# Kernel tuning notes

Hardware: AMD Instinct MI355X
Metric: run time of the kernel (lower is better)

The kernel has to match this reference:

```python
import jax, jax.numpy as jnp
import numpy as np

N_WORD = 50000
N_DOC = 10000
E_WW = 800000
E_WD = 320000


def _sage(h_src, h_dst, src, dst, n_dst, W_self, W_neigh, b):
    # DGL SAGEConv('mean'): fc_self(h_dst) + fc_neigh(mean_{u in N(v)} h_u) + bias
    ones = jnp.ones((src.shape[0],), dtype=h_src.dtype)
    deg = jax.ops.segment_sum(ones, dst, num_segments=n_dst)            # [n_dst]
    agg = jax.ops.segment_sum(h_src[src], dst, num_segments=n_dst)      # [n_dst, d]
    mean = agg / jnp.maximum(deg, 1.0)[:, None]                          # zero for isolated
    return h_dst @ W_self + mean @ W_neigh + b


def _layer(xw, xd, edges, Ws, Wn, b):
    (ww_s, ww_d, wwr_s, wwr_d, wd_s, wd_d, wdr_s, wdr_d) = edges
    # relations targeting 'word': word2word, word2wordr, word2documentr
    h_ww = _sage(xw, xw, ww_s, ww_d, N_WORD, Ws[0], Wn[0], b[0])
    h_wwr = _sage(xw, xw, wwr_s, wwr_d, N_WORD, Ws[1], Wn[1], b[1])
    h_wdr = _sage(xd, xw, wdr_s, wdr_d, N_WORD, Ws[3], Wn[3], b[3])
    # relation targeting 'document': word2document
    h_wd = _sage(xw, xd, wd_s, wd_d, N_DOC, Ws[2], Wn[2], b[2])
    # HeteroGraphConv aggregate='stack' then torch.sum(dim=1) == sum over relations; then relu
    return jax.nn.relu(h_ww + h_wwr + h_wdr), jax.nn.relu(h_wd)


def setup_inputs() -> dict:
    key = jax.random.key(0)
    ks = jax.random.split(key, 20)
    d_in, d_h = 256, 128
    inp = {
        "x_word": jax.random.normal(ks[0], (N_WORD, d_in), jnp.float32),
        "x_doc": jax.random.normal(ks[1], (N_DOC, d_in), jnp.float32),
        "ww_src": jax.random.randint(ks[2], (E_WW,), 0, N_WORD, jnp.int32),
        "ww_dst": jax.random.randint(ks[3], (E_WW,), 0, N_WORD, jnp.int32),
        "wwr_src": jax.random.randint(ks[4], (E_WW,), 0, N_WORD, jnp.int32),
        "wwr_dst": jax.random.randint(ks[5], (E_WW,), 0, N_WORD, jnp.int32),
        "wd_src": jax.random.randint(ks[6], (E_WD,), 0, N_WORD, jnp.int32),
        "wd_dst": jax.random.randint(ks[7], (E_WD,), 0, N_DOC, jnp.int32),
        "wdr_src": jax.random.randint(ks[8], (E_WD,), 0, N_DOC, jnp.int32),
        "wdr_dst": jax.random.randint(ks[9], (E_WD,), 0, N_WORD, jnp.int32),
        "Wself1": jax.random.normal(ks[10], (4, d_in, d_h), jnp.float32) * (1.0 / np.sqrt(d_in)),
        "Wneigh1": jax.random.normal(ks[11], (4, d_in, d_h), jnp.float32) * (1.0 / np.sqrt(d_in)),
        "b1": jnp.zeros((4, d_h), jnp.float32),
        "Wself2": jax.random.normal(ks[12], (4, d_h, d_h), jnp.float32) * (1.0 / np.sqrt(d_h)),
        "Wneigh2": jax.random.normal(ks[13], (4, d_h, d_h), jnp.float32) * (1.0 / np.sqrt(d_h)),
        "b2": jnp.zeros((4, d_h), jnp.float32),
        "lin_w": jax.random.normal(ks[14], (1, d_h), jnp.float32) * (1.0 / np.sqrt(d_h)),
        "lin_b": jnp.ones((1,), jnp.float32),
    }
    return inp


def reference(x_word, x_doc, ww_src, ww_dst, wwr_src, wwr_dst, wd_src, wd_dst,
              wdr_src, wdr_dst, Wself1, Wneigh1, b1, Wself2, Wneigh2, b2, lin_w, lin_b):
    edges = (ww_src, ww_dst, wwr_src, wwr_dst, wd_src, wd_dst, wdr_src, wdr_dst)
    xw, xd = _layer(x_word, x_doc, edges, Wself1, Wneigh1, b1)
    xw, xd = _layer(xw, xd, edges, Wself2, Wneigh2, b2)
    out_w = jax.nn.sigmoid(xw @ lin_w.T + lin_b)  # [N_WORD, 1]
    out_d = jax.nn.sigmoid(xd @ lin_w.T + lin_b)  # [N_DOC, 1]
    return out_w, out_d
```

## Files before the change

### kernel.cpp

```cpp
#include <hip/hip_runtime.h>
#include <math.h>

#define N_WORD 50000
#define N_DOC  10000
#define E_WW   800000
#define E_WD   320000
#define D_IN   256
#define D_H    128

#define NPB    256
#define NBK_W  196
#define NBK_D  40
#define BKT    (3 * NBK_W + NBK_D)
#define EPB    8192
#define NBLK_WW 98
#define NBLK_WD 40
#define NBLK_TOT (2 * NBLK_WW + 2 * NBLK_WD)
#define PACK_BLKS 145

#define CAP_WW  4736
#define CAP_WDR 2176
#define CAP_WD  8960

#define WSTRIP ((N_WORD + 63) / 64)
#define DSTRIP ((N_DOC + 63) / 64)
#define NSTRIP (WSTRIP + DSTRIP)

typedef __attribute__((ext_vector_type(8))) short short8;
typedef __attribute__((ext_vector_type(4))) float f32x4;

__device__ inline unsigned short f2bf(float f) {
  unsigned u = __float_as_uint(f);
  u = (u + 0x7fffu + ((u >> 16) & 1u)) >> 16;
  return (unsigned short)u;
}

__device__ inline float bflo(unsigned u) { return __uint_as_float(u << 16); }
__device__ inline float bfhi(unsigned u) { return __uint_as_float(u & 0xffff0000u); }

struct G6 { const short* B[6]; unsigned short* C[6]; };

template <int ABF, int K>
__device__ void gemm_body(const void* __restrict__ Aw, const void* __restrict__ Ad,
                          const G6& g, int blk) {
  constexpr int KT = K >> 5;
  int wid = threadIdx.x >> 6, lane = threadIdx.x & 63;
  const void* A; int M, row0, h0, h1;
  if (blk < WSTRIP) { A = Aw; M = N_WORD; row0 = blk << 6; h0 = 0; h1 = 4; }
  else { A = Ad; M = N_DOC; row0 = (blk - WSTRIP) << 6; h0 = 4; h1 = 6; }
  int r = lane & 15, quad = lane >> 4;
  int m0 = row0 + wid * 16;
  int mA = m0 + r; if (mA >= M) mA = M - 1;
  short8 afr[KT];
  if (ABF) {
    const short* ap = (const short*)A + (size_t)mA * K + quad * 8;
#pragma unroll
    for (int kt = 0; kt < KT; ++kt) afr[kt] = *(const short8*)(ap + kt * 32);
  } else {
    const float* ap = (const float*)A + (size_t)mA * K + quad * 8;
#pragma unroll
    for (int kt = 0; kt < KT; ++kt) {
      float4 a0 = *(const float4*)(ap + kt * 32);
      float4 a1 = *(const float4*)(ap + kt * 32 + 4);
      short8 v;
      v[0] = (short)f2bf(a0.x); v[1] = (short)f2bf(a0.y);
      v[2] = (short)f2bf(a0.z); v[3] = (short)f2bf(a0.w);
      v[4] = (short)f2bf(a1.x); v[5] = (short)f2bf(a1.y);
      v[6] = (short)f2bf(a1.z); v[7] = (short)f2bf(a1.w);
      afr[kt] = v;
    }
  }
  for (int h = h0; h < h1; ++h) {
    const short* Bp = g.B[h];
    f32x4 acc[8];
#pragma unroll
    for (int nt = 0; nt < 8; ++nt) acc[nt] = (f32x4){0.f, 0.f, 0.f, 0.f};
#pragma unroll
    for (int kt = 0; kt < KT; ++kt) {
      const short* bbase = Bp + ((size_t)kt * 4096) + lane * 8;
#pragma unroll
      for (int nt = 0; nt < 8; ++nt) {
        short8 bf = *(const short8*)(bbase + (size_t)nt * 512);
        acc[nt] = __builtin_amdgcn_mfma_f32_16x16x32_bf16(afr[kt], bf, acc[nt], 0, 0, 0);
      }
    }
    unsigned short* C = g.C[h];
#pragma unroll
    for (int nt = 0; nt < 8; ++nt)
#pragma unroll
      for (int rr = 0; rr < 4; ++rr) {
        int row = m0 + quad * 4 + rr;
        if (row < M) C[(size_t)row * 128 + nt * 16 + r] = f2bf(acc[nt][rr]);
      }
  }
}

__global__ __launch_bounds__(256) void prep_kernel(
    const float* __restrict__ Ws1, const float* __restrict__ Wn1,
    const float* __restrict__ Ws2, const float* __restrict__ Wn2,
    short* __restrict__ Bp1, short* __restrict__ Bp2,
    const float* __restrict__ b1, const float* __restrict__ b2,
    float* __restrict__ bs1, float* __restrict__ bs2, int* __restrict__ bcnt,
    unsigned* __restrict__ zA, unsigned* __restrict__ zB,
    unsigned* __restrict__ zC, unsigned* __restrict__ zD) {
  int b = blockIdx.x;
  if (b == PACK_BLKS) {
    for (int i = threadIdx.x; i < BKT; i += 256) bcnt[i] = 0;
    if (threadIdx.x < 64) {
      zA[(size_t)N_WORD * 64 + threadIdx.x] = 0;
      zB[(size_t)N_WORD * 64 + threadIdx.x] = 0;
      zC[(size_t)N_WORD * 64 + threadIdx.x] = 0;
      zD[(size_t)N_DOC * 64 + threadIdx.x] = 0;
    }
    return;
  }
  int tid = b * 256 + threadIdx.x;
  const int L1T = 6 * 4096;
  const int L2T = 6 * 2048;
  if (tid >= L1T + L2T) {
    int t = tid - (L1T + L2T);
    if (t < 128) bs1[t] = b1[t] + b1[128 + t] + b1[384 + t];
    else if (t < 256) { int u = t - 128; bs2[u] = b2[u] + b2[128 + u] + b2[384 + u]; }
    return;
  }
  const float *src0, *src1 = nullptr, *src2 = nullptr;
  short* dstp;
  int kt, nt, lane;
  if (tid < L1T) {
    int mat = tid / 4096, rem = tid % 4096;
    kt = rem / 512; nt = (rem / 64) % 8; lane = rem % 64;
    const int W1 = 256 * 128;
    if (mat == 0) { src0 = Ws1; src1 = Ws1 + W1; src2 = Ws1 + 3 * W1; }
    else if (mat <= 4) src0 = Wn1 + (size_t)(mat - 1) * W1;
    else src0 = Ws1 + 2 * W1;
    dstp = Bp1 + (size_t)mat * W1 + ((size_t)(kt * 8 + nt) * 64 + lane) * 8;
  } else {
    int t2 = tid - L1T;
    int mat = t2 / 2048, rem = t2 % 2048;
    kt = rem / 512; nt = (rem / 64) % 8; lane = rem % 64;
    const int W2 = 128 * 128;
    if (mat == 0) { src0 = Ws2; src1 = Ws2 + W2; src2 = Ws2 + 3 * W2; }
    else if (mat <= 4) src0 = Wn2 + (size_t)(mat - 1) * W2;
    else src0 = Ws2 + 2 * W2;
    dstp = Bp2 + (size_t)mat * W2 + ((size_t)(kt * 8 + nt) * 64 + lane) * 8;
  }
  int n = nt * 16 + (lane & 15);
  int kb = kt * 32 + (lane >> 4) * 8;
  short8 v;
#pragma unroll
  for (int j = 0; j < 8; ++j) {
    float f = src0[(size_t)(kb + j) * 128 + n];
    if (src1) f += src1[(size_t)(kb + j) * 128 + n] + src2[(size_t)(kb + j) * 128 + n];
    v[j] = (short)f2bf(f);
  }
  *(short8*)dstp = v;
}

__device__ inline void rel_map(int b, const int* wwd, const int* wwrd, const int* wdrd,
                               const int* wdd, const int*& dst, int& E, int& gbase, int& lb) {
  if (b < NBLK_WW) { dst = wwd; E = E_WW; gbase = 0; lb = b; }
  else if (b < 2 * NBLK_WW) { dst = wwrd; E = E_WW; gbase = NBK_W; lb = b - NBLK_WW; }
  else if (b < 2 * NBLK_WW + NBLK_WD) { dst = wdrd; E = E_WD; gbase = 2 * NBK_W; lb = b - 2 * NBLK_WW; }
  else { dst = wdd; E = E_WD; gbase = 3 * NBK_W; lb = b - 2 * NBLK_WW - NBLK_WD; }
}

struct BinLDS {
  unsigned buf[EPB];
  int hist[NBK_W];
  int lofs[NBK_W];
  int gofs[NBK_W];
  int lcur[NBK_W];
  int sm[256];
};

__global__ __launch_bounds__(256, 4) void bin_gemm1(
    const int* wws, const int* wwd, const int* wwrs, const int* wwrd,
    const int* wdrs, const int* wdrd, const int* wds, const int* wdd,
    int* bcnt, unsigned* st_ww, unsigned* st_wwr, unsigned* st_wdr, unsigned* st_wd,
    const float* __restrict__ Aw, const float* __restrict__ Ad, G6 g) {
  __shared__ BinLDS L;
  int b = blockIdx.x;
  if (b >= NBLK_TOT) {
    gemm_body<0, 256>(Aw, Ad, g, b - NBLK_TOT);
    return;
  }
  const int* dst; int E, gbase, lb;
  rel_map(b, wwd, wwrd, wdrd, wdd, dst, E, gbase, lb);
  const int* src; unsigned* st; int cap;
  if (b < NBLK_WW) { src = wws; st = st_ww; cap = CAP_WW; }
  else if (b < 2 * NBLK_WW) { src = wwrs; st = st_wwr; cap = CAP_WW; }
  else if (b < 2 * NBLK_WW + NBLK_WD) { src = wdrs; st = st_wdr; cap = CAP_WDR; }
  else { src = wds; st = st_wd; cap = CAP_WD; }
  int tid = threadIdx.x;
  int e0 = lb * EPB;
  int ecnt = E - e0; if (ecnt > EPB) ecnt = EPB;
  if (tid < NBK_W) L.hist[tid] = 0;
  __syncthreads();
  int dcache[EPB / 256];
#pragma unroll
  for (int k = 0; k < EPB / 256; ++k) {
    int i = e0 + k * 256 + tid;
    int d = (i < E) ? dst[i] : -1;
    dcache[k] = d;
    if (d >= 0) atomicAdd(&L.hist[d >> 8], 1);
  }
  __syncthreads();
  {
    int v = (tid < NBK_W) ? L.hist[tid] : 0;
    L.sm[tid] = v;
    __syncthreads();
    for (int o = 1; o < 256; o <<= 1) {
      int add = (tid >= o) ? L.sm[tid - o] : 0;
      __syncthreads();
      L.sm[tid] += add;
      __syncthreads();
    }
    if (tid < NBK_W) {
      int ex = L.sm[tid] - v;
      L.lofs[tid] = ex;
      L.lcur[tid] = ex;
      int base = v ? atomicAdd(&bcnt[gbase + tid], v) : 0;
      L.gofs[tid] = (int)((size_t)tid * cap) + base - ex;
    }
  }
  __syncthreads();
#pragma unroll
  for (int k = 0; k < EPB / 256; ++k) {
    int d = dcache[k];
    if (d >= 0) {
      int i = e0 + k * 256 + tid;
      int bk = d >> 8;
      int p = atomicAdd(&L.lcur[bk], 1);
      L.buf[p] = ((unsigned)bk << 24) | ((unsigned)(d & 255) << 16) |
                 (unsigned)(src[i] & 0xFFFF);
    }
  }
  __syncthreads();
#pragma unroll
  for (int k = 0; k < EPB / 256; ++k) {
    int p = k * 256 + tid;
    if (p < ecnt) {
      unsigned e = L.buf[p];
      st[L.gofs[e >> 24] + p] = e & 0x00FFFFFFu;
    }
  }
}

struct CSRB {
  const unsigned *st_ww, *st_wwr, *st_wdr, *st_wd;
  unsigned short *c_ww, *c_wwr, *c_wdr, *c_wd;
  int *rp_ww, *rp_wwr, *rp_wdr, *rp_wd;
  const int* bcnt;
};

__global__ __launch_bounds__(256) void place_kernel(CSRB q) {
  __shared__ int cnt[256], off[256], sm[256];
  int g = blockIdx.x;
  const unsigned* st; unsigned short* csr; int* rp; int relFirst, relLast, n, cap, Etot;
  if (g < NBK_W)            { st = q.st_ww;  csr = q.c_ww;  rp = q.rp_ww;  relFirst = 0;         relLast = NBK_W - 1;     n = N_WORD; cap = CAP_WW;  Etot = E_WW; }
  else if (g < 2 * NBK_W)   { st = q.st_wwr; csr = q.c_wwr; rp = q.rp_wwr; relFirst = NBK_W;     relLast = 2 * NBK_W - 1; n = N_WORD; cap = CAP_WW;  Etot = E_WW; }
  else if (g < 3 * NBK_W)   { st = q.st_wdr; csr = q.c_wdr; rp = q.rp_wdr; relFirst = 2 * NBK_W; relLast = 3 * NBK_W - 1; n = N_WORD; cap = CAP_WDR; Etot = E_WD; }
  else                      { st = q.st_wd;  csr = q.c_wd;  rp = q.rp_wd;  relFirst = 3 * NBK_W; relLast = BKT - 1;       n = N_DOC;  cap = CAP_WD;  Etot = E_WD; }
  int cb = g - relFirst;
  int tid = threadIdx.x;
  int v = (tid < cb) ? q.bcnt[relFirst + tid] : 0;
  sm[tid] = v;
  __syncthreads();
  for (int o = 128; o > 0; o >>= 1) {
    if (tid < o) sm[tid] += sm[tid + o];
    __syncthreads();
  }
  int bstart = sm[0];
  if (g == relLast && tid == 0) rp[n] = Etot;
  __syncthreads();
  int node_base = cb << 8;
  int node_cnt = n - node_base; if (node_cnt > NPB) node_cnt = NPB;
  int ecnt = q.bcnt[g];
  const unsigned* w = st + (size_t)cb * cap;
  cnt[tid] = 0;
  __syncthreads();
  for (int j = tid; j < ecnt; j += 256) atomicAdd(&cnt[w[j] >> 16], 1);
  __syncthreads();
  int c = cnt[tid];
  sm[tid] = c;
  __syncthreads();
  for (int o = 1; o < 256; o <<= 1) {
    int add = (tid >= o) ? sm[tid - o] : 0;
    __syncthreads();
    sm[tid] += add;
    __syncthreads();
  }
  int ex = sm[tid] - c;
  off[tid] = ex;
  if (tid < node_cnt) rp[node_base + tid] = bstart + ex;
  __syncthreads();
  for (int j = tid; j < ecnt; j += 256) {
    unsigned e = w[j];
    int p = atomicAdd(&off[e >> 16], 1);
    csr[bstart + p] = (unsigned short)(e & 0xFFFFu);
  }
}

__global__ __launch_bounds__(256, 6) void gemm2_kernel(
    const void* __restrict__ Aw, const void* __restrict__ Ad, G6 g) {
  gemm_body<1, 128>(Aw, Ad, g, blockIdx.x);
}

__device__ inline void accum_rel4(const uint4* __restrict__ Y,
                                  const unsigned short* __restrict__ csr,
                                  int beg, int end, int lane, int r, int g,
                                  int zrow, float* __restrict__ f) {
  int deg = end - beg;
  if (deg <= 0) return;
  float a[8];
#pragma unroll
  for (int i = 0; i < 8; ++i) a[i] = 0.f;
  for (int base = beg; base < end; base += 64) {
    int cnt = end - base; if (cnt > 64) cnt = 64;
    int ld = base + lane; if (ld >= end) ld = end - 1;
    int idx = csr[ld];
    for (int j = 0; j < cnt; j += 16) {
      uint4 u[4];
#pragma unroll
      for (int t = 0; t < 4; ++t) {
        int e = j + (t << 2) + g;
        int sel = (e < cnt) ? e : 0;
        int sv = __shfl(idx, sel, 64);
        int s = (e < cnt) ? sv : zrow;
        u[t] = Y[(unsigned)((s << 4) + r)];
      }
#pragma unroll
      for (int t = 0; t < 4; ++t) {
        a[0] += bflo(u[t].x); a[1] += bfhi(u[t].x);
        a[2] += bflo(u[t].y); a[3] += bfhi(u[t].y);
        a[4] += bflo(u[t].z); a[5] += bfhi(u[t].z);
        a[6] += bflo(u[t].w); a[7] += bfhi(u[t].w);
      }
    }
  }
  float inv = 1.0f / (float)deg;
#pragma unroll
  for (int i = 0; i < 8; ++i) f[i] += a[i] * inv;
}

__global__ __launch_bounds__(256) void gather_all(
    const unsigned* __restrict__ y_ww, const unsigned* __restrict__ y_wwr,
    const unsigned* __restrict__ y_wdr, const unsigned* __restrict__ y_wd,
    const unsigned short* __restrict__ c_ww, const unsigned short* __restrict__ c_wwr,
    const unsigned short* __restrict__ c_wdr, const unsigned short* __restrict__ c_wd,
    const int* __restrict__ r_ww, const int* __restrict__ r_wwr,
    const int* __restrict__ r_wdr, const int* __restrict__ r_wd,
    const unsigned* __restrict__ tW, const unsigned* __restrict__ tD,
    const float* __restrict__ bW, const float* __restrict__ bD,
    const float* __restrict__ lw, const float* __restrict__ lb,
    unsigned* __restrict__ oW16, unsigned* __restrict__ oD16,
    float* __restrict__ oF, int mode) {
  int gn = (blockIdx.x << 2) + (threadIdx.x >> 6);
  if (gn >= N_WORD + N_DOC) return;
  int lane = threadIdx.x & 63;
  int r = lane & 15, g = lane >> 4;
  float f[8];
#pragma unroll
  for (int i = 0; i < 8; ++i) f[i] = 0.f;
  bool isw = (gn < N_WORD);
  int node = isw ? gn : gn - N_WORD;
  if (isw) {
    accum_rel4((const uint4*)y_ww, c_ww, r_ww[node], r_ww[node + 1], lane, r, g, N_WORD, f);
    accum_rel4((const uint4*)y_wwr, c_wwr, r_wwr[node], r_wwr[node + 1], lane, r, g, N_WORD, f);
    accum_rel4((const uint4*)y_wdr, c_wdr, r_wdr[node], r_wdr[node + 1], lane, r, g, N_DOC, f);
  } else {
    accum_rel4((const uint4*)y_wd, c_wd, r_wd[node], r_wd[node + 1], lane, r, g, N_WORD, f);
  }
#pragma unroll
  for (int i = 0; i < 8; ++i) {
    f[i] += __shfl_xor(f[i], 16, 64);
    f[i] += __shfl_xor(f[i], 32, 64);
  }
  const unsigned* tS = isw ? tW : tD;
  uint4 tu = ((const uint4*)tS)[(unsigned)((node << 4) + r)];
  const float* bs = isw ? bW : bD;
  float4 bv0 = ((const float4*)bs)[2 * r];
  float4 bv1 = ((const float4*)bs)[2 * r + 1];
  f[0] = fmaxf(f[0] + bflo(tu.x) + bv0.x, 0.f);
  f[1] = fmaxf(f[1] + bfhi(tu.x) + bv0.y, 0.f);
  f[2] = fmaxf(f[2] + bflo(tu.y) + bv0.z, 0.f);
  f[3] = fmaxf(f[3] + bfhi(tu.y) + bv0.w, 0.f);
  f[4] = fmaxf(f[4] + bflo(tu.z) + bv1.x, 0.f);
  f[5] = fmaxf(f[5] + bfhi(tu.z) + bv1.y, 0.f);
  f[6] = fmaxf(f[6] + bflo(tu.w) + bv1.z, 0.f);
  f[7] = fmaxf(f[7] + bfhi(tu.w) + bv1.w, 0.f);
  if (mode == 1) {
    if (g == 0) {
      uint4 pk;
      pk.x = (unsigned)f2bf(f[0]) | ((unsigned)f2bf(f[1]) << 16);
      pk.y = (unsigned)f2bf(f[2]) | ((unsigned)f2bf(f[3]) << 16);
      pk.z = (unsigned)f2bf(f[4]) | ((unsigned)f2bf(f[5]) << 16);
      pk.w = (unsigned)f2bf(f[6]) | ((unsigned)f2bf(f[7]) << 16);
      unsigned* o = isw ? oW16 : oD16;
      ((uint4*)o)[(unsigned)((node << 4) + r)] = pk;
    }
  } else {
    float4 lv0 = ((const float4*)lw)[2 * r];
    float4 lv1 = ((const float4*)lw)[2 * r + 1];
    float s = f[0] * lv0.x + f[1] * lv0.y + f[2] * lv0.z + f[3] * lv0.w +
              f[4] * lv1.x + f[5] * lv1.y + f[6] * lv1.z + f[7] * lv1.w;
#pragma unroll
    for (int off = 8; off > 0; off >>= 1) s += __shfl_xor(s, off, 64);
    if (lane == 0) oF[isw ? node : N_WORD + node] = 1.0f / (1.0f + expf(-(s + lb[0])));
  }
}

extern "C" void kernel_launch(void* const* d_in, const int* in_sizes, int n_in,
                              void* d_out, int out_size, void* d_ws, size_t ws_size,
                              hipStream_t stream) {
  const float* xw      = (const float*)d_in[0];
  const float* xd      = (const float*)d_in[1];
  const int*   ww_src  = (const int*)d_in[2];
  const int*   ww_dst  = (const int*)d_in[3];
  const int*   wwr_src = (const int*)d_in[4];
  const int*   wwr_dst = (const int*)d_in[5];
  const int*   wd_src  = (const int*)d_in[6];
  const int*   wd_dst  = (const int*)d_in[7];
  const int*   wdr_src = (const int*)d_in[8];
  const int*   wdr_dst = (const int*)d_in[9];
  const float* Ws1     = (const float*)d_in[10];
  const float* Wn1     = (const float*)d_in[11];
  const float* b1      = (const float*)d_in[12];
  const float* Ws2     = (const float*)d_in[13];
  const float* Wn2     = (const float*)d_in[14];
  const float* b2      = (const float*)d_in[15];
  const float* lin_w   = (const float*)d_in[16];
  const float* lin_b   = (const float*)d_in[17];
  float* out = (float*)d_out;

  char* p = (char*)d_ws;
  auto alloc = [&](size_t nbytes) {
    char* r = p;
    p += (nbytes + 255) & ~(size_t)255;
    return r;
  };
  unsigned* twA  = (unsigned*)alloc((size_t)N_WORD * D_H * 2);
  unsigned* tdA  = (unsigned*)alloc((size_t)N_DOC * D_H * 2);
  unsigned* xw1B = (unsigned*)alloc((size_t)N_WORD * D_H * 2 + 256);
  unsigned* xd1B = (unsigned*)alloc((size_t)N_DOC * D_H * 2);
  unsigned* yB0 = (unsigned*)alloc((size_t)N_WORD * D_H * 2);
  unsigned* yB1 = (unsigned*)alloc(((size_t)NBK_W * CAP_WDR + (size_t)NBK_D * CAP_WD) * 4);
  unsigned* yB2 = (unsigned*)alloc((size_t)N_WORD * D_H * 2 + 256);
  unsigned* ydB = (unsigned*)alloc((size_t)N_DOC * D_H * 2 + 256);
  unsigned short* csr_ww  = (unsigned short*)alloc((size_t)E_WW * 2);
  unsigned short* csr_wwr = (unsigned short*)alloc((size_t)E_WW * 2);
  unsigned short* csr_wdr = (unsigned short*)alloc((size_t)E_WD * 2);
  unsigned short* csr_wd  = (unsigned short*)alloc((size_t)E_WD * 2);
  int* rp_ww  = (int*)alloc((size_t)(N_WORD + 1) * 4);
  int* rp_wwr = (int*)alloc((size_t)(N_WORD + 1) * 4);
  int* rp_wdr = (int*)alloc((size_t)(N_WORD + 1) * 4);
  int* rp_wd  = (int*)alloc((size_t)(N_DOC + 1) * 4);
  short* Bp1 = (short*)alloc((size_t)6 * 256 * 128 * 2);
  short* Bp2 = (short*)alloc((size_t)6 * 128 * 128 * 2);
  int* bcnt  = (int*)alloc((size_t)BKT * 4);
  float* bs1 = (float*)alloc(D_H * 4);
  float* bs2 = (float*)alloc(D_H * 4);
  unsigned* yBX = (unsigned*)alloc((size_t)N_WORD * D_H * 2 + 256);
  unsigned* st_ww  = yB0;
  unsigned* st_wwr = st_ww + (size_t)NBK_W * CAP_WW;
  unsigned* st_wdr = yB1;
  unsigned* st_wd  = st_wdr + (size_t)NBK_W * CAP_WDR;

  const int W1 = 256 * 128;
  const int W2 = 128 * 128;

  prep_kernel<<<PACK_BLKS + 1, 256, 0, stream>>>(
      Ws1, Wn1, Ws2, Wn2, Bp1, Bp2, b1, b2, bs1, bs2, bcnt,
      yB2, xw1B, yBX, ydB);

  G6 g1;
  g1.B[0] = Bp1 + 0 * W1; g1.C[0] = (unsigned short*)twA;
  g1.B[1] = Bp1 + 1 * W1; g1.C[1] = (unsigned short*)yB2;
  g1.B[2] = Bp1 + 2 * W1; g1.C[2] = (unsigned short*)xw1B;
  g1.B[3] = Bp1 + 3 * W1; g1.C[3] = (unsigned short*)yBX;
  g1.B[4] = Bp1 + 5 * W1; g1.C[4] = (unsigned short*)tdA;
  g1.B[5] = Bp1 + 4 * W1; g1.C[5] = (unsigned short*)ydB;
  bin_gemm1<<<NBLK_TOT + NSTRIP, 256, 0, stream>>>(
      ww_src, ww_dst, wwr_src, wwr_dst, wdr_src, wdr_dst, wd_src, wd_dst,
      bcnt, st_ww, st_wwr, st_wdr, st_wd, xw, xd, g1);

  CSRB q;
  q.st_ww = st_ww; q.st_wwr = st_wwr; q.st_wdr = st_wdr; q.st_wd = st_wd;
  q.c_ww = csr_ww; q.c_wwr = csr_wwr; q.c_wdr = csr_wdr; q.c_wd = csr_wd;
  q.rp_ww = rp_ww; q.rp_wwr = rp_wwr; q.rp_wdr = rp_wdr; q.rp_wd = rp_wd;
  q.bcnt = bcnt;
  place_kernel<<<BKT, 256, 0, stream>>>(q);

  gather_all<<<(N_WORD + N_DOC + 3) / 4, 256, 0, stream>>>(
      yB2, xw1B, ydB, yBX, csr_ww, csr_wwr, csr_wdr, csr_wd,
      rp_ww, rp_wwr, rp_wdr, rp_wd, twA, tdA, bs1, b1 + 256,
      lin_w, lin_b, yB0, xd1B, nullptr, 1);

  G6 g2;
  g2.B[0] = Bp2 + 0 * W2; g2.C[0] = (unsigned short*)twA;
  g2.B[1] = Bp2 + 1 * W2; g2.C[1] = (unsigned short*)yB2;
  g2.B[2] = Bp2 + 2 * W2; g2.C[2] = (unsigned short*)xw1B;
  g2.B[3] = Bp2 + 3 * W2; g2.C[3] = (unsigned short*)yBX;
  g2.B[4] = Bp2 + 5 * W2; g2.C[4] = (unsigned short*)tdA;
  g2.B[5] = Bp2 + 4 * W2; g2.C[5] = (unsigned short*)ydB;
  gemm2_kernel<<<NSTRIP, 256, 0, stream>>>(yB0, xd1B, g2);

  gather_all<<<(N_WORD + N_DOC + 3) / 4, 256, 0, stream>>>(
      yB2, xw1B, ydB, yBX, csr_ww, csr_wwr, csr_wdr, csr_wd,
      rp_ww, rp_wwr, rp_wdr, rp_wd, twA, tdA, bs2, b2 + 256,
      lin_w, lin_b, nullptr, nullptr, out, 2);
}
```

Baseline: 385.8 us.

## Move edge binning into prep kernel and split GEMM1 into its own kernel

Edge binning moves out of the combined bin/GEMM1 kernel and into the weight-packing prep kernel, and layer-1 GEMM becomes a standalone kernel with launch bounds of 2 waves per EU. The bucket counter is now cleared with a memset instead of inside the prep kernel. The aim is to stop the large LDS footprint of binning from limiting occupancy of the GEMM, and to let the GEMM run without binning blocks mixed in. The gather loop drops per-element bounds selects by loading a zero row for out-of-range lanes, and accumulates in float2 vectors so the compiler can use packed adds. It adds an extra memset launch, and the prep kernel now carries the binning LDS allocation.

```diff
diff --git a/kernel.cpp b/kernel.cpp
--- a/kernel.cpp
+++ b/kernel.cpp
@@ -28,6 +28,7 @@
 
 typedef __attribute__((ext_vector_type(8))) short short8;
 typedef __attribute__((ext_vector_type(4))) float f32x4;
+typedef __attribute__((ext_vector_type(2))) float f32x2;
 
 __device__ inline unsigned short f2bf(float f) {
   unsigned u = __float_as_uint(f);
@@ -70,6 +71,8 @@
       afr[kt] = v;
     }
   }
+#pragma unroll
+  for (int kt = 0; kt < KT; ++kt) asm volatile("" : "+v"(afr[kt]));
   for (int h = h0; h < h1; ++h) {
     const short* Bp = g.B[h];
     f32x4 acc[8];
@@ -95,17 +98,118 @@
   }
 }
 
-__global__ __launch_bounds__(256) void prep_kernel(
+__global__ __launch_bounds__(256, 2) void gemm1_kernel(
+    const void* __restrict__ Aw, const void* __restrict__ Ad, G6 g) {
+  gemm_body<0, 256>(Aw, Ad, g, blockIdx.x);
+}
+
+__global__ __launch_bounds__(256, 2) void gemm2_kernel(
+    const void* __restrict__ Aw, const void* __restrict__ Ad, G6 g) {
+  gemm_body<1, 128>(Aw, Ad, g, blockIdx.x);
+}
+
+__device__ inline void rel_map(int b, const int* wwd, const int* wwrd, const int* wdrd,
+                               const int* wdd, const int*& dst, int& E, int& gbase, int& lb) {
+  if (b < NBLK_WW) { dst = wwd; E = E_WW; gbase = 0; lb = b; }
+  else if (b < 2 * NBLK_WW) { dst = wwrd; E = E_WW; gbase = NBK_W; lb = b - NBLK_WW; }
+  else if (b < 2 * NBLK_WW + NBLK_WD) { dst = wdrd; E = E_WD; gbase = 2 * NBK_W; lb = b - 2 * NBLK_WW; }
+  else { dst = wdd; E = E_WD; gbase = 3 * NBK_W; lb = b - 2 * NBLK_WW - NBLK_WD; }
+}
+
+struct BinLDS {
+  unsigned buf[EPB];
+  int hist[NBK_W];
+  int lofs[NBK_W];
+  int gofs[NBK_W];
+  int lcur[NBK_W];
+  int sm[256];
+};
+
+__device__ void bin_body(int b, BinLDS& L,
+    const int* wws, const int* wwd, const int* wwrs, const int* wwrd,
+    const int* wdrs, const int* wdrd, const int* wds, const int* wdd,
+    int* bcnt, unsigned* st_ww, unsigned* st_wwr, unsigned* st_wdr, unsigned* st_wd) {
+  const int* dst; int E, gbase, lb;
+  rel_map(b, wwd, wwrd, wdrd, wdd, dst, E, gbase, lb);
+  const int* src; unsigned* st; int cap;
+  if (b < NBLK_WW) { src = wws; st = st_ww; cap = CAP_WW; }
+  else if (b < 2 * NBLK_WW) { src = wwrs; st = st_wwr; cap = CAP_WW; }
+  else if (b < 2 * NBLK_WW + NBLK_WD) { src = wdrs; st = st_wdr; cap = CAP_WDR; }
+  else { src = wds; st = st_wd; cap = CAP_WD; }
+  int tid = threadIdx.x;
+  int e0 = lb * EPB;
+  int ecnt = E - e0; if (ecnt > EPB) ecnt = EPB;
+  if (tid < NBK_W) L.hist[tid] = 0;
+  __syncthreads();
+  int dcache[EPB / 256];
+#pragma unroll
+  for (int k = 0; k < EPB / 256; ++k) {
+    int i = e0 + k * 256 + tid;
+    int d = (i < E) ? dst[i] : -1;
+    dcache[k] = d;
+    if (d >= 0) atomicAdd(&L.hist[d >> 8], 1);
+  }
+  __syncthreads();
+  {
+    int v = (tid < NBK_W) ? L.hist[tid] : 0;
+    L.sm[tid] = v;
+    __syncthreads();
+    for (int o = 1; o < 256; o <<= 1) {
+      int add = (tid >= o) ? L.sm[tid - o] : 0;
+      __syncthreads();
+      L.sm[tid] += add;
+      __syncthreads();
+    }
+    if (tid < NBK_W) {
+      int ex = L.sm[tid] - v;
+      L.lofs[tid] = ex;
+      L.lcur[tid] = ex;
+      int base = v ? atomicAdd(&bcnt[gbase + tid], v) : 0;
+      L.gofs[tid] = (int)((size_t)tid * cap) + base - ex;
+    }
+  }
+  __syncthreads();
+#pragma unroll
+  for (int k = 0; k < EPB / 256; ++k) {
+    int d = dcache[k];
+    if (d >= 0) {
+      int i = e0 + k * 256 + tid;
+      int bk = d >> 8;
+      int p = atomicAdd(&L.lcur[bk], 1);
+      L.buf[p] = ((unsigned)bk << 24) | ((unsigned)(d & 255) << 16) |
+                 (unsigned)(src[i] & 0xFFFF);
+    }
+  }
+  __syncthreads();
+#pragma unroll
+  for (int k = 0; k < EPB / 256; ++k) {
+    int p = k * 256 + tid;
+    if (p < ecnt) {
+      unsigned e = L.buf[p];
+      st[L.gofs[e >> 24] + p] = e & 0x00FFFFFFu;
+    }
+  }
+}
+
+__global__ __launch_bounds__(256, 4) void prepbin_kernel(
     const float* __restrict__ Ws1, const float* __restrict__ Wn1,
     const float* __restrict__ Ws2, const float* __restrict__ Wn2,
     short* __restrict__ Bp1, short* __restrict__ Bp2,
     const float* __restrict__ b1, const float* __restrict__ b2,
-    float* __restrict__ bs1, float* __restrict__ bs2, int* __restrict__ bcnt,
+    float* __restrict__ bs1, float* __restrict__ bs2,
     unsigned* __restrict__ zA, unsigned* __restrict__ zB,
-    unsigned* __restrict__ zC, unsigned* __restrict__ zD) {
+    unsigned* __restrict__ zC, unsigned* __restrict__ zD,
+    const int* wws, const int* wwd, const int* wwrs, const int* wwrd,
+    const int* wdrs, const int* wdrd, const int* wds, const int* wdd,
+    int* bcnt, unsigned* st_ww, unsigned* st_wwr, unsigned* st_wdr, unsigned* st_wd) {
+  __shared__ BinLDS L;
   int b = blockIdx.x;
+  if (b > PACK_BLKS) {
+    bin_body(b - PACK_BLKS - 1, L, wws, wwd, wwrs, wwrd, wdrs, wdrd, wds, wdd,
+             bcnt, st_ww, st_wwr, st_wdr, st_wd);
+    return;
+  }
   if (b == PACK_BLKS) {
-    for (int i = threadIdx.x; i < BKT; i += 256) bcnt[i] = 0;
     if (threadIdx.x < 64) {
       zA[(size_t)N_WORD * 64 + threadIdx.x] = 0;
       zB[(size_t)N_WORD * 64 + threadIdx.x] = 0;
@@ -156,96 +260,6 @@
   *(short8*)dstp = v;
 }
 
-__device__ inline void rel_map(int b, const int* wwd, const int* wwrd, const int* wdrd,
-                               const int* wdd, const int*& dst, int& E, int& gbase, int& lb) {
-  if (b < NBLK_WW) { dst = wwd; E = E_WW; gbase = 0; lb = b; }
-  else if (b < 2 * NBLK_WW) { dst = wwrd; E = E_WW; gbase = NBK_W; lb = b - NBLK_WW; }
-  else if (b < 2 * NBLK_WW + NBLK_WD) { dst = wdrd; E = E_WD; gbase = 2 * NBK_W; lb = b - 2 * NBLK_WW; }
-  else { dst = wdd; E = E_WD; gbase = 3 * NBK_W; lb = b - 2 * NBLK_WW - NBLK_WD; }
-}
-
-struct BinLDS {
-  unsigned buf[EPB];
-  int hist[NBK_W];
-  int lofs[NBK_W];
-  int gofs[NBK_W];
-  int lcur[NBK_W];
-  int sm[256];
-};
-
-__global__ __launch_bounds__(256, 4) void bin_gemm1(
-    const int* wws, const int* wwd, const int* wwrs, const int* wwrd,
-    const int* wdrs, const int* wdrd, const int* wds, const int* wdd,
-    int* bcnt, unsigned* st_ww, unsigned* st_wwr, unsigned* st_wdr, unsigned* st_wd,
-    const float* __restrict__ Aw, const float* __restrict__ Ad, G6 g) {
-  __shared__ BinLDS L;
-  int b = blockIdx.x;
-  if (b >= NBLK_TOT) {
-    gemm_body<0, 256>(Aw, Ad, g, b - NBLK_TOT);
-    return;
-  }
-  const int* dst; int E, gbase, lb;
-  rel_map(b, wwd, wwrd, wdrd, wdd, dst, E, gbase, lb);
-  const int* src; unsigned* st; int cap;
-  if (b < NBLK_WW) { src = wws; st = st_ww; cap = CAP_WW; }
-  else if (b < 2 * NBLK_WW) { src = wwrs; st = st_wwr; cap = CAP_WW; }
-  else if (b < 2 * NBLK_WW + NBLK_WD) { src = wdrs; st = st_wdr; cap = CAP_WDR; }
-  else { src = wds; st = st_wd; cap = CAP_WD; }
-  int tid = threadIdx.x;
-  int e0 = lb * EPB;
-  int ecnt = E - e0; if (ecnt > EPB) ecnt = EPB;
-  if (tid < NBK_W) L.hist[tid] = 0;
-  __syncthreads();
-  int dcache[EPB / 256];
-#pragma unroll
-  for (int k = 0; k < EPB / 256; ++k) {
-    int i = e0 + k * 256 + tid;
-    int d = (i < E) ? dst[i] : -1;
-    dcache[k] = d;
-    if (d >= 0) atomicAdd(&L.hist[d >> 8], 1);
-  }
-  __syncthreads();
-  {
-    int v = (tid < NBK_W) ? L.hist[tid] : 0;
-    L.sm[tid] = v;
-    __syncthreads();
-    for (int o = 1; o < 256; o <<= 1) {
-      int add = (tid >= o) ? L.sm[tid - o] : 0;
-      __syncthreads();
-      L.sm[tid] += add;
-      __syncthreads();
-    }
-    if (tid < NBK_W) {
-      int ex = L.sm[tid] - v;
-      L.lofs[tid] = ex;
-      L.lcur[tid] = ex;
-      int base = v ? atomicAdd(&bcnt[gbase + tid], v) : 0;
-      L.gofs[tid] = (int)((size_t)tid * cap) + base - ex;
-    }
-  }
-  __syncthreads();
-#pragma unroll
-  for (int k = 0; k < EPB / 256; ++k) {
-    int d = dcache[k];
-    if (d >= 0) {
-      int i = e0 + k * 256 + tid;
-      int bk = d >> 8;
-      int p = atomicAdd(&L.lcur[bk], 1);
-      L.buf[p] = ((unsigned)bk << 24) | ((unsigned)(d & 255) << 16) |
-                 (unsigned)(src[i] & 0xFFFF);
-    }
-  }
-  __syncthreads();
-#pragma unroll
-  for (int k = 0; k < EPB / 256; ++k) {
-    int p = k * 256 + tid;
-    if (p < ecnt) {
-      unsigned e = L.buf[p];
-      st[L.gofs[e >> 24] + p] = e & 0x00FFFFFFu;
-    }
-  }
-}
-
 struct CSRB {
   const unsigned *st_ww, *st_wwr, *st_wdr, *st_wd;
   unsigned short *c_ww, *c_wwr, *c_wdr, *c_wd;
@@ -301,46 +315,35 @@
   }
 }
 
-__global__ __launch_bounds__(256, 6) void gemm2_kernel(
-    const void* __restrict__ Aw, const void* __restrict__ Ad, G6 g) {
-  gemm_body<1, 128>(Aw, Ad, g, blockIdx.x);
-}
-
 __device__ inline void accum_rel4(const uint4* __restrict__ Y,
                                   const unsigned short* __restrict__ csr,
                                   int beg, int end, int lane, int r, int g,
-                                  int zrow, float* __restrict__ f) {
+                                  int zrow, f32x2* __restrict__ f) {
   int deg = end - beg;
   if (deg <= 0) return;
-  float a[8];
-#pragma unroll
-  for (int i = 0; i < 8; ++i) a[i] = 0.f;
+  f32x2 a0 = {0.f, 0.f}, a1 = a0, a2 = a0, a3 = a0;
   for (int base = beg; base < end; base += 64) {
     int cnt = end - base; if (cnt > 64) cnt = 64;
-    int ld = base + lane; if (ld >= end) ld = end - 1;
-    int idx = csr[ld];
+    int ld = base + lane;
+    int idx = (ld < end) ? (int)csr[ld] : zrow;
     for (int j = 0; j < cnt; j += 16) {
       uint4 u[4];
 #pragma unroll
       for (int t = 0; t < 4; ++t) {
-        int e = j + (t << 2) + g;
-        int sel = (e < cnt) ? e : 0;
-        int sv = __shfl(idx, sel, 64);
-        int s = (e < cnt) ? sv : zrow;
-        u[t] = Y[(unsigned)((s << 4) + r)];
+        int sv = __shfl(idx, j + (t << 2) + g, 64);
+        u[t] = Y[(unsigned)((sv << 4) + r)];
       }
 #pragma unroll
       for (int t = 0; t < 4; ++t) {
-        a[0] += bflo(u[t].x); a[1] += bfhi(u[t].x);
-        a[2] += bflo(u[t].y); a[3] += bfhi(u[t].y);
-        a[4] += bflo(u[t].z); a[5] += bfhi(u[t].z);
-        a[6] += bflo(u[t].w); a[7] += bfhi(u[t].w);
+        a0 += (f32x2){bflo(u[t].x), bfhi(u[t].x)};
+        a1 += (f32x2){bflo(u[t].y), bfhi(u[t].y)};
+        a2 += (f32x2){bflo(u[t].z), bfhi(u[t].z)};
+        a3 += (f32x2){bflo(u[t].w), bfhi(u[t].w)};
       }
     }
   }
   float inv = 1.0f / (float)deg;
-#pragma unroll
-  for (int i = 0; i < 8; ++i) f[i] += a[i] * inv;
+  f[0] += a0 * inv; f[1] += a1 * inv; f[2] += a2 * inv; f[3] += a3 * inv;
 }
 
 __global__ __launch_bounds__(256) void gather_all(
@@ -359,9 +362,9 @@
   if (gn >= N_WORD + N_DOC) return;
   int lane = threadIdx.x & 63;
   int r = lane & 15, g = lane >> 4;
-  float f[8];
-#pragma unroll
-  for (int i = 0; i < 8; ++i) f[i] = 0.f;
+  f32x2 f[4];
+#pragma unroll
+  for (int i = 0; i < 4; ++i) f[i] = (f32x2){0.f, 0.f};
   bool isw = (gn < N_WORD);
   int node = isw ? gn : gn - N_WORD;
   if (isw) {
@@ -372,38 +375,40 @@
     accum_rel4((const uint4*)y_wd, c_wd, r_wd[node], r_wd[node + 1], lane, r, g, N_WORD, f);
   }
 #pragma unroll
-  for (int i = 0; i < 8; ++i) {
-    f[i] += __shfl_xor(f[i], 16, 64);
-    f[i] += __shfl_xor(f[i], 32, 64);
+  for (int i = 0; i < 4; ++i) {
+    f[i].x += __shfl_xor(f[i].x, 16, 64);
+    f[i].y += __shfl_xor(f[i].y, 16, 64);
+    f[i].x += __shfl_xor(f[i].x, 32, 64);
+    f[i].y += __shfl_xor(f[i].y, 32, 64);
   }
   const unsigned* tS = isw ? tW : tD;
   uint4 tu = ((const uint4*)tS)[(unsigned)((node << 4) + r)];
   const float* bs = isw ? bW : bD;
   float4 bv0 = ((const float4*)bs)[2 * r];
   float4 bv1 = ((const float4*)bs)[2 * r + 1];
-  f[0] = fmaxf(f[0] + bflo(tu.x) + bv0.x, 0.f);
-  f[1] = fmaxf(f[1] + bfhi(tu.x) + bv0.y, 0.f);
-  f[2] = fmaxf(f[2] + bflo(tu.y) + bv0.z, 0.f);
-  f[3] = fmaxf(f[3] + bfhi(tu.y) + bv0.w, 0.f);
-  f[4] = fmaxf(f[4] + bflo(tu.z) + bv1.x, 0.f);
-  f[5] = fmaxf(f[5] + bfhi(tu.z) + bv1.y, 0.f);
-  f[6] = fmaxf(f[6] + bflo(tu.w) + bv1.z, 0.f);
-  f[7] = fmaxf(f[7] + bfhi(tu.w) + bv1.w, 0.f);
+  f[0].x = fmaxf(f[0].x + bflo(tu.x) + bv0.x, 0.f);
+  f[0].y = fmaxf(f[0].y + bfhi(tu.x) + bv0.y, 0.f);
+  f[1].x = fmaxf(f[1].x + bflo(tu.y) + bv0.z, 0.f);
+  f[1].y = fmaxf(f[1].y + bfhi(tu.y) + bv0.w, 0.f);
+  f[2].x = fmaxf(f[2].x + bflo(tu.z) + bv1.x, 0.f);
+  f[2].y = fmaxf(f[2].y + bfhi(tu.z) + bv1.y, 0.f);
+  f[3].x = fmaxf(f[3].x + bflo(tu.w) + bv1.z, 0.f);
+  f[3].y = fmaxf(f[3].y + bfhi(tu.w) + bv1.w, 0.f);
   if (mode == 1) {
     if (g == 0) {
       uint4 pk;
-      pk.x = (unsigned)f2bf(f[0]) | ((unsigned)f2bf(f[1]) << 16);
-      pk.y = (unsigned)f2bf(f[2]) | ((unsigned)f2bf(f[3]) << 16);
-      pk.z = (unsigned)f2bf(f[4]) | ((unsigned)f2bf(f[5]) << 16);
-      pk.w = (unsigned)f2bf(f[6]) | ((unsigned)f2bf(f[7]) << 16);
+      pk.x = (unsigned)f2bf(f[0].x) | ((unsigned)f2bf(f[0].y) << 16);
+      pk.y = (unsigned)f2bf(f[1].x) | ((unsigned)f2bf(f[1].y) << 16);
+      pk.z = (unsigned)f2bf(f[2].x) | ((unsigned)f2bf(f[2].y) << 16);
+      pk.w = (unsigned)f2bf(f[3].x) | ((unsigned)f2bf(f[3].y) << 16);
       unsigned* o = isw ? oW16 : oD16;
       ((uint4*)o)[(unsigned)((node << 4) + r)] = pk;
     }
   } else {
     float4 lv0 = ((const float4*)lw)[2 * r];
     float4 lv1 = ((const float4*)lw)[2 * r + 1];
-    float s = f[0] * lv0.x + f[1] * lv0.y + f[2] * lv0.z + f[3] * lv0.w +
-              f[4] * lv1.x + f[5] * lv1.y + f[6] * lv1.z + f[7] * lv1.w;
+    float s = f[0].x * lv0.x + f[0].y * lv0.y + f[1].x * lv0.z + f[1].y * lv0.w +
+              f[2].x * lv1.x + f[2].y * lv1.y + f[3].x * lv1.z + f[3].y * lv1.w;
 #pragma unroll
     for (int off = 8; off > 0; off >>= 1) s += __shfl_xor(s, off, 64);
     if (lane == 0) oF[isw ? node : N_WORD + node] = 1.0f / (1.0f + expf(-(s + lb[0])));
@@ -469,9 +474,13 @@
   const int W1 = 256 * 128;
   const int W2 = 128 * 128;
 
-  prep_kernel<<<PACK_BLKS + 1, 256, 0, stream>>>(
-      Ws1, Wn1, Ws2, Wn2, Bp1, Bp2, b1, b2, bs1, bs2, bcnt,
-      yB2, xw1B, yBX, ydB);
+  hipMemsetAsync(bcnt, 0, (size_t)BKT * 4, stream);
+
+  prepbin_kernel<<<PACK_BLKS + 1 + NBLK_TOT, 256, 0, stream>>>(
+      Ws1, Wn1, Ws2, Wn2, Bp1, Bp2, b1, b2, bs1, bs2,
+      yB2, xw1B, yBX, ydB,
+      ww_src, ww_dst, wwr_src, wwr_dst, wdr_src, wdr_dst, wd_src, wd_dst,
+      bcnt, st_ww, st_wwr, st_wdr, st_wd);
 
   G6 g1;
   g1.B[0] = Bp1 + 0 * W1; g1.C[0] = (unsigned short*)twA;
@@ -480,9 +489,7 @@
   g1.B[3] = Bp1 + 3 * W1; g1.C[3] = (unsigned short*)yBX;
   g1.B[4] = Bp1 + 5 * W1; g1.C[4] = (unsigned short*)tdA;
   g1.B[5] = Bp1 + 4 * W1; g1.C[5] = (unsigned short*)ydB;
-  bin_gemm1<<<NBLK_TOT + NSTRIP, 256, 0, stream>>>(
-      ww_src, ww_dst, wwr_src, wwr_dst, wdr_src, wdr_dst, wd_src, wd_dst,
-      bcnt, st_ww, st_wwr, st_wdr, st_wd, xw, xd, g1);
+  gemm1_kernel<<<NSTRIP, 256, 0, stream>>>(xw, xd, g1);
 
   CSRB q;
   q.st_ww = st_ww; q.st_wwr = st_wwr; q.st_wdr = st_wdr; q.st_wd = st_wd;
```

Measured after the change: 406.3 us. 1.05x slower.
